# Performance work log

Measured on AMD Instinct MI355X. Metric: run time of the kernel, lower is better.

Reference implementation:

```python
import jax, jax.numpy as jnp
import numpy as np

B, S, H = 4, 2048, 1024
EXP_BITS, SIG_BITS = 5, 10  # rmode=1 -> round-to-nearest


def quantize(x):
    """Simulated low-precision float quantization (LightChop-style) with STE.

    exp_bits exponent bits (bias = 2^(e-1)-1, exponent clamped -> subnormal
    handling falls out of the clamp), sig_bits significand bits, round-to-nearest.
    """
    bias = 2 ** (EXP_BITS - 1) - 1
    ax = jnp.abs(x)
    e = jnp.floor(jnp.log2(jnp.where(ax > 0, ax, 1.0)))
    e = jnp.clip(e, 1 - bias, bias)               # clamp to representable exponent range
    scale = jnp.exp2(e - SIG_BITS)                # ulp at this exponent
    q = jnp.round(x / scale) * scale              # round significand to SIG_BITS bits
    max_val = (2.0 - 2.0 ** (-SIG_BITS)) * 2.0 ** bias
    q = jnp.clip(q, -max_val, max_val)            # saturate overflow
    # straight-through estimator: forward = q, backward = identity
    return x + jax.lax.stop_gradient(q - x)


def setup_inputs() -> dict:
    key = jax.random.key(0)
    ks = jax.random.split(key, 7)
    w_scale = 1.0 / np.sqrt(H)
    return {
        "x": jax.random.normal(ks[0], (B, S, H), dtype=jnp.float32),
        "Wq": jax.random.normal(ks[1], (H, H), dtype=jnp.float32) * w_scale,
        "bq": jax.random.normal(ks[2], (H,), dtype=jnp.float32) * 0.01,
        "Wk": jax.random.normal(ks[3], (H, H), dtype=jnp.float32) * w_scale,
        "bk": jax.random.normal(ks[4], (H,), dtype=jnp.float32) * 0.01,
        "Wv": jax.random.normal(ks[5], (H, H), dtype=jnp.float32) * w_scale,
        "bv": jax.random.normal(ks[6], (H,), dtype=jnp.float32) * 0.01,
    }


def reference(x, Wq, bq, Wk, bk, Wv, bv):
    # nn.Linear: y = x @ W.T + b   (W stored [out, in])
    q = quantize(jnp.einsum("bsh,oh->bso", x, Wq) + bq)
    k = quantize(jnp.einsum("bsh,oh->bso", x, Wk) + bk)
    v = quantize(jnp.einsum("bsh,oh->bso", x, Wv) + bv)
    inv_sqrt_h = 1.0 / (H ** 0.5)
    scores = quantize(jnp.einsum("bsh,bth->bst", q, k) * inv_sqrt_h)  # [B,S,S]
    attn = quantize(jax.nn.softmax(scores, axis=-1))
    return jnp.einsum("bst,bth->bsh", attn, v)
```

## Files before the change

kernel.cpp:

```cpp
#include <hip/hip_runtime.h>
#include <hip/hip_fp16.h>

#define B_ 4
#define S_ 2048
#define H_ 1024
#define M_ (B_ * S_)

typedef _Float16 f16;
typedef _Float16 f16x8 __attribute__((ext_vector_type(8)));
typedef _Float16 f16x4 __attribute__((ext_vector_type(4)));
typedef float f32x4 __attribute__((ext_vector_type(4)));

typedef __attribute__((address_space(3))) unsigned int* lds_u32p;
typedef const __attribute__((address_space(1))) unsigned int* gbl_u32p;

__device__ __forceinline__ void stage16(const f16* g, f16* l) {
  __builtin_amdgcn_global_load_lds((gbl_u32p)g, (lds_u32p)l, 16, 0, 0);
}

__global__ __launch_bounds__(256) void downconvert_all(
    const float* __restrict__ x, const float* __restrict__ W0,
    const float* __restrict__ W1, const float* __restrict__ W2,
    f16* __restrict__ xh, f16* __restrict__ Wh) {
  const int b = blockIdx.x;
  const float* src;
  f16* dst;
  long i;
  if (b < M_ * H_ / 1024) {
    src = x; dst = xh;
    i = (long)b * 256 + threadIdx.x;
  } else {
    const int wb = b - M_ * H_ / 1024;
    const int sel = wb >> 10;
    src = sel == 0 ? W0 : (sel == 1 ? W1 : W2);
    dst = Wh + (long)sel * H_ * H_;
    i = (long)(wb & 1023) * 256 + threadIdx.x;
  }
  f32x4 v = ((const f32x4*)src)[i];
  f16x4 h;
#pragma unroll
  for (int c = 0; c < 4; c++) h[c] = (f16)v[c];
  ((f16x4*)dst)[i] = h;
}

__global__ __launch_bounds__(256, 2)
void qkv_gemm(const f16* __restrict__ xh, const f16* __restrict__ Wh,
              const float* __restrict__ bq, const float* __restrict__ bk,
              const float* __restrict__ bv, f16* __restrict__ qkv,
              f16* __restrict__ vT) {
  __shared__ __align__(16) f16 As[2 * 128 * 32];
  __shared__ __align__(16) f16 Bs[2 * 128 * 32];
  const int t = threadIdx.x;
  const int wave = t >> 6, lane = t & 63;
  const int quad = lane >> 4, l16 = lane & 15;
  const int wm = (wave & 1) * 64, wn = (wave >> 1) * 64;
  const int sel = blockIdx.y >> 3;
  const int ntile = (blockIdx.y & 7) * 128;
  const int mtile = blockIdx.x * 128;

  const f16* Ab = xh + (long)mtile * H_;
  const f16* Bb = Wh + (long)sel * H_ * H_ + (long)ntile * H_;

  const int r0 = t >> 2;
  const int c8 = (t & 3) * 8;

  f32x4 acc[4][4] = {};

  for (int k0 = 0; k0 < H_; k0 += 64) {
    __syncthreads();
    stage16(Ab + (long)r0 * H_ + k0 + c8,             As + t * 8);
    stage16(Ab + (long)(r0 + 64) * H_ + k0 + c8,      As + 2048 + t * 8);
    stage16(Ab + (long)r0 * H_ + k0 + 32 + c8,        As + 4096 + t * 8);
    stage16(Ab + (long)(r0 + 64) * H_ + k0 + 32 + c8, As + 6144 + t * 8);
    stage16(Bb + (long)r0 * H_ + k0 + c8,             Bs + t * 8);
    stage16(Bb + (long)(r0 + 64) * H_ + k0 + c8,      Bs + 2048 + t * 8);
    stage16(Bb + (long)r0 * H_ + k0 + 32 + c8,        Bs + 4096 + t * 8);
    stage16(Bb + (long)(r0 + 64) * H_ + k0 + 32 + c8, Bs + 6144 + t * 8);
    __syncthreads();
#pragma unroll
    for (int kk = 0; kk < 2; kk++) {
      f16x8 ah[4], bh[4];
#pragma unroll
      for (int i = 0; i < 4; i++) {
        ah[i] = *(const f16x8*)&As[kk * 4096 + (wm + i * 16 + l16) * 32 + quad * 8];
        bh[i] = *(const f16x8*)&Bs[kk * 4096 + (wn + i * 16 + l16) * 32 + quad * 8];
      }
#pragma unroll
      for (int i = 0; i < 4; i++)
#pragma unroll
        for (int j = 0; j < 4; j++)
          acc[i][j] = __builtin_amdgcn_mfma_f32_16x16x32_f16(ah[i], bh[j], acc[i][j], 0, 0, 0);
    }
  }

  const float* bias = sel == 0 ? bq : (sel == 1 ? bk : bv);
  if (sel == 2) {
#pragma unroll
    for (int j = 0; j < 4; j++) {
      int n = ntile + wn + j * 16 + l16;
      float bb = bias[n];
#pragma unroll
      for (int i = 0; i < 4; i++) {
        int m = mtile + wm + i * 16 + quad * 4;
        f16x4 pack;
#pragma unroll
        for (int r = 0; r < 4; r++) pack[r] = (f16)(acc[i][j][r] + bb);
        *(f16x4*)&vT[((long)(m >> 11) * H_ + n) * S_ + (m & 2047)] = pack;
      }
    }
  } else {
    f16* out = qkv + (long)sel * M_ * H_;
#pragma unroll
    for (int j = 0; j < 4; j++) {
      int n = ntile + wn + j * 16 + l16;
      float bb = bias[n];
#pragma unroll
      for (int i = 0; i < 4; i++) {
        int m = mtile + wm + i * 16 + quad * 4;
#pragma unroll
        for (int r = 0; r < 4; r++)
          out[(long)(m + r) * H_ + n] = (f16)(acc[i][j][r] + bb);
      }
    }
  }
}

template <int OUT_F16>
__global__ __launch_bounds__(256, 2)
void gemm_nt(const f16* __restrict__ A, const f16* __restrict__ Bm,
             void* __restrict__ C, int lda, int ldb, int ldc, int K,
             long sA, long sB, long sC, float alpha) {
  __shared__ __align__(16) f16 As[2 * 128 * 32];
  __shared__ __align__(16) f16 Bs[2 * 128 * 32];
  const int t = threadIdx.x;
  const int wave = t >> 6, lane = t & 63;
  const int quad = lane >> 4, l16 = lane & 15;
  const int wm = (wave & 1) * 64, wn = (wave >> 1) * 64;
  const f16* Ab = A + blockIdx.z * sA + (long)blockIdx.x * 128 * lda;
  const f16* Bb = Bm + blockIdx.z * sB + (long)blockIdx.y * 128 * ldb;
  const int r0 = t >> 2, c8 = (t & 3) * 8;
  f32x4 acc[4][4] = {};
  for (int k0 = 0; k0 < K; k0 += 64) {
    __syncthreads();
    stage16(Ab + (long)r0 * lda + k0 + c8,             As + t * 8);
    stage16(Ab + (long)(r0 + 64) * lda + k0 + c8,      As + 2048 + t * 8);
    stage16(Ab + (long)r0 * lda + k0 + 32 + c8,        As + 4096 + t * 8);
    stage16(Ab + (long)(r0 + 64) * lda + k0 + 32 + c8, As + 6144 + t * 8);
    stage16(Bb + (long)r0 * ldb + k0 + c8,             Bs + t * 8);
    stage16(Bb + (long)(r0 + 64) * ldb + k0 + c8,      Bs + 2048 + t * 8);
    stage16(Bb + (long)r0 * ldb + k0 + 32 + c8,        Bs + 4096 + t * 8);
    stage16(Bb + (long)(r0 + 64) * ldb + k0 + 32 + c8, Bs + 6144 + t * 8);
    __syncthreads();
#pragma unroll
    for (int kk = 0; kk < 2; kk++) {
      f16x8 af[4], bf[4];
#pragma unroll
      for (int i = 0; i < 4; i++) {
        af[i] = *(const f16x8*)&As[kk * 4096 + (wm + i * 16 + l16) * 32 + quad * 8];
        bf[i] = *(const f16x8*)&Bs[kk * 4096 + (wn + i * 16 + l16) * 32 + quad * 8];
      }
#pragma unroll
      for (int i = 0; i < 4; i++)
#pragma unroll
        for (int j = 0; j < 4; j++)
          acc[i][j] = __builtin_amdgcn_mfma_f32_16x16x32_f16(af[i], bf[j], acc[i][j], 0, 0, 0);
    }
  }
  const long mb = (long)blockIdx.x * 128 + wm;
  const long nb = (long)blockIdx.y * 128 + wn;
#pragma unroll
  for (int i = 0; i < 4; i++)
#pragma unroll
    for (int j = 0; j < 4; j++) {
      long m = mb + i * 16 + quad * 4;
      long n = nb + j * 16 + l16;
#pragma unroll
      for (int r = 0; r < 4; r++) {
        float v = acc[i][j][r] * alpha;
        if (OUT_F16)
          ((f16*)C)[blockIdx.z * sC + (m + r) * ldc + n] = (f16)v;
        else
          ((float*)C)[blockIdx.z * sC + (m + r) * ldc + n] = v;
      }
    }
}

__global__ __launch_bounds__(256) void softmax_q(f16* __restrict__ sc) {
  const long row = blockIdx.x;
  f16* p = sc + row * S_;
  const int t = threadIdx.x;
  const int wave = t >> 6, lane = t & 63;
  f16x8 v = ((const f16x8*)p)[t];
  float f[8];
  float m = -3.0e38f;
#pragma unroll
  for (int c = 0; c < 8; c++) { f[c] = (float)v[c]; m = fmaxf(m, f[c]); }
#pragma unroll
  for (int o = 32; o > 0; o >>= 1) m = fmaxf(m, __shfl_xor(m, o));
  __shared__ float redm[4], reds[4];
  if (lane == 0) redm[wave] = m;
  __syncthreads();
  m = fmaxf(fmaxf(redm[0], redm[1]), fmaxf(redm[2], redm[3]));
  float s = 0.f, e[8];
#pragma unroll
  for (int c = 0; c < 8; c++) { e[c] = __expf(f[c] - m); s += e[c]; }
#pragma unroll
  for (int o = 32; o > 0; o >>= 1) s += __shfl_xor(s, o);
  if (lane == 0) reds[wave] = s;
  __syncthreads();
  s = reds[0] + reds[1] + reds[2] + reds[3];
  float inv = 1.0f / s;
  f16x8 ov;
#pragma unroll
  for (int c = 0; c < 8; c++) ov[c] = (f16)(e[c] * inv);
  ((f16x8*)p)[t] = ov;
}

extern "C" void kernel_launch(void* const* d_in, const int* in_sizes, int n_in,
                              void* d_out, int out_size, void* d_ws, size_t ws_size,
                              hipStream_t stream) {
  (void)in_sizes; (void)n_in; (void)out_size; (void)ws_size;
  const float* x  = (const float*)d_in[0];
  const float* Wq = (const float*)d_in[1];
  const float* bq = (const float*)d_in[2];
  const float* Wk = (const float*)d_in[3];
  const float* bk = (const float*)d_in[4];
  const float* Wv = (const float*)d_in[5];
  const float* bv = (const float*)d_in[6];

  char* ws = (char*)d_ws;
  f16* xh  = (f16*)ws; ws += (size_t)M_ * H_ * 2;
  f16* Wh  = (f16*)ws; ws += (size_t)3 * H_ * H_ * 2;
  f16* qkv = (f16*)ws; ws += (size_t)2 * M_ * H_ * 2;
  f16* vT  = (f16*)ws; ws += (size_t)B_ * H_ * S_ * 2;
  f16* sc  = (f16*)ws; ws += (size_t)B_ * S_ * S_ * 2;

  downconvert_all<<<M_ * H_ / 1024 + 3 * H_ * H_ / 1024, 256, 0, stream>>>(
      x, Wq, Wk, Wv, xh, Wh);

  qkv_gemm<<<dim3(64, 24), 256, 0, stream>>>(xh, Wh, bq, bk, bv, qkv, vT);

  gemm_nt<1><<<dim3(16, 16, 4), 256, 0, stream>>>(
      qkv, qkv + (size_t)M_ * H_, sc, H_, H_, S_, H_,
      (long)S_ * H_, (long)S_ * H_, (long)S_ * S_, 0.03125f);

  softmax_q<<<M_, 256, 0, stream>>>(sc);

  gemm_nt<0><<<dim3(16, 8, 4), 256, 0, stream>>>(
      sc, vT, d_out, S_, S_, H_, S_,
      (long)S_ * S_, (long)H_ * S_, (long)S_ * H_, 1.0f);
}
```

Baseline: 252.0 us.

## Fuse all stages into one persistent kernel with global atomic barriers

```diff
diff --git a/kernel.cpp b/kernel.cpp
--- a/kernel.cpp
+++ b/kernel.cpp
@@ -5,6 +5,7 @@
 #define S_ 2048
 #define H_ 1024
 #define M_ (B_ * S_)
+#define NBLK 512
 
 typedef _Float16 f16;
 typedef _Float16 f16x8 __attribute__((ext_vector_type(8)));
@@ -18,126 +19,26 @@
   __builtin_amdgcn_global_load_lds((gbl_u32p)g, (lds_u32p)l, 16, 0, 0);
 }
 
-__global__ __launch_bounds__(256) void downconvert_all(
-    const float* __restrict__ x, const float* __restrict__ W0,
-    const float* __restrict__ W1, const float* __restrict__ W2,
-    f16* __restrict__ xh, f16* __restrict__ Wh) {
-  const int b = blockIdx.x;
-  const float* src;
-  f16* dst;
-  long i;
-  if (b < M_ * H_ / 1024) {
-    src = x; dst = xh;
-    i = (long)b * 256 + threadIdx.x;
-  } else {
-    const int wb = b - M_ * H_ / 1024;
-    const int sel = wb >> 10;
-    src = sel == 0 ? W0 : (sel == 1 ? W1 : W2);
-    dst = Wh + (long)sel * H_ * H_;
-    i = (long)(wb & 1023) * 256 + threadIdx.x;
-  }
-  f32x4 v = ((const f32x4*)src)[i];
-  f16x4 h;
-#pragma unroll
-  for (int c = 0; c < 4; c++) h[c] = (f16)v[c];
-  ((f16x4*)dst)[i] = h;
-}
-
-__global__ __launch_bounds__(256, 2)
-void qkv_gemm(const f16* __restrict__ xh, const f16* __restrict__ Wh,
-              const float* __restrict__ bq, const float* __restrict__ bk,
-              const float* __restrict__ bv, f16* __restrict__ qkv,
-              f16* __restrict__ vT) {
-  __shared__ __align__(16) f16 As[2 * 128 * 32];
-  __shared__ __align__(16) f16 Bs[2 * 128 * 32];
-  const int t = threadIdx.x;
+__device__ __forceinline__ void gsync(unsigned* bar, unsigned target) {
+  __syncthreads();
+  if (threadIdx.x == 0) {
+    __hip_atomic_fetch_add(bar, 1u, __ATOMIC_ACQ_REL, __HIP_MEMORY_SCOPE_AGENT);
+    while (__hip_atomic_load(bar, __ATOMIC_ACQUIRE, __HIP_MEMORY_SCOPE_AGENT) < target)
+      __builtin_amdgcn_s_sleep(8);
+  }
+  __syncthreads();
+}
+
+template <int OUT_F16>
+__device__ __forceinline__ void gemm_tile(
+    const f16* __restrict__ A, const f16* __restrict__ Bm, void* __restrict__ C,
+    int lda, int ldb, int ldc, int K, long sA, long sB, long sC, float alpha,
+    int bx, int by, int bz, int t, f16* As, f16* Bs) {
   const int wave = t >> 6, lane = t & 63;
   const int quad = lane >> 4, l16 = lane & 15;
   const int wm = (wave & 1) * 64, wn = (wave >> 1) * 64;
-  const int sel = blockIdx.y >> 3;
-  const int ntile = (blockIdx.y & 7) * 128;
-  const int mtile = blockIdx.x * 128;
-
-  const f16* Ab = xh + (long)mtile * H_;
-  const f16* Bb = Wh + (long)sel * H_ * H_ + (long)ntile * H_;
-
-  const int r0 = t >> 2;
-  const int c8 = (t & 3) * 8;
-
-  f32x4 acc[4][4] = {};
-
-  for (int k0 = 0; k0 < H_; k0 += 64) {
-    __syncthreads();
-    stage16(Ab + (long)r0 * H_ + k0 + c8,             As + t * 8);
-    stage16(Ab + (long)(r0 + 64) * H_ + k0 + c8,      As + 2048 + t * 8);
-    stage16(Ab + (long)r0 * H_ + k0 + 32 + c8,        As + 4096 + t * 8);
-    stage16(Ab + (long)(r0 + 64) * H_ + k0 + 32 + c8, As + 6144 + t * 8);
-    stage16(Bb + (long)r0 * H_ + k0 + c8,             Bs + t * 8);
-    stage16(Bb + (long)(r0 + 64) * H_ + k0 + c8,      Bs + 2048 + t * 8);
-    stage16(Bb + (long)r0 * H_ + k0 + 32 + c8,        Bs + 4096 + t * 8);
-    stage16(Bb + (long)(r0 + 64) * H_ + k0 + 32 + c8, Bs + 6144 + t * 8);
-    __syncthreads();
-#pragma unroll
-    for (int kk = 0; kk < 2; kk++) {
-      f16x8 ah[4], bh[4];
-#pragma unroll
-      for (int i = 0; i < 4; i++) {
-        ah[i] = *(const f16x8*)&As[kk * 4096 + (wm + i * 16 + l16) * 32 + quad * 8];
-        bh[i] = *(const f16x8*)&Bs[kk * 4096 + (wn + i * 16 + l16) * 32 + quad * 8];
-      }
-#pragma unroll
-      for (int i = 0; i < 4; i++)
-#pragma unroll
-        for (int j = 0; j < 4; j++)
-          acc[i][j] = __builtin_amdgcn_mfma_f32_16x16x32_f16(ah[i], bh[j], acc[i][j], 0, 0, 0);
-    }
-  }
-
-  const float* bias = sel == 0 ? bq : (sel == 1 ? bk : bv);
-  if (sel == 2) {
-#pragma unroll
-    for (int j = 0; j < 4; j++) {
-      int n = ntile + wn + j * 16 + l16;
-      float bb = bias[n];
-#pragma unroll
-      for (int i = 0; i < 4; i++) {
-        int m = mtile + wm + i * 16 + quad * 4;
-        f16x4 pack;
-#pragma unroll
-        for (int r = 0; r < 4; r++) pack[r] = (f16)(acc[i][j][r] + bb);
-        *(f16x4*)&vT[((long)(m >> 11) * H_ + n) * S_ + (m & 2047)] = pack;
-      }
-    }
-  } else {
-    f16* out = qkv + (long)sel * M_ * H_;
-#pragma unroll
-    for (int j = 0; j < 4; j++) {
-      int n = ntile + wn + j * 16 + l16;
-      float bb = bias[n];
-#pragma unroll
-      for (int i = 0; i < 4; i++) {
-        int m = mtile + wm + i * 16 + quad * 4;
-#pragma unroll
-        for (int r = 0; r < 4; r++)
-          out[(long)(m + r) * H_ + n] = (f16)(acc[i][j][r] + bb);
-      }
-    }
-  }
-}
-
-template <int OUT_F16>
-__global__ __launch_bounds__(256, 2)
-void gemm_nt(const f16* __restrict__ A, const f16* __restrict__ Bm,
-             void* __restrict__ C, int lda, int ldb, int ldc, int K,
-             long sA, long sB, long sC, float alpha) {
-  __shared__ __align__(16) f16 As[2 * 128 * 32];
-  __shared__ __align__(16) f16 Bs[2 * 128 * 32];
-  const int t = threadIdx.x;
-  const int wave = t >> 6, lane = t & 63;
-  const int quad = lane >> 4, l16 = lane & 15;
-  const int wm = (wave & 1) * 64, wn = (wave >> 1) * 64;
-  const f16* Ab = A + blockIdx.z * sA + (long)blockIdx.x * 128 * lda;
-  const f16* Bb = Bm + blockIdx.z * sB + (long)blockIdx.y * 128 * ldb;
+  const f16* Ab = A + bz * sA + (long)bx * 128 * lda;
+  const f16* Bb = Bm + bz * sB + (long)by * 128 * ldb;
   const int r0 = t >> 2, c8 = (t & 3) * 8;
   f32x4 acc[4][4] = {};
   for (int k0 = 0; k0 < K; k0 += 64) {
@@ -166,8 +67,8 @@
           acc[i][j] = __builtin_amdgcn_mfma_f32_16x16x32_f16(af[i], bf[j], acc[i][j], 0, 0, 0);
     }
   }
-  const long mb = (long)blockIdx.x * 128 + wm;
-  const long nb = (long)blockIdx.y * 128 + wn;
+  const long mb = (long)bx * 128 + wm;
+  const long nb = (long)by * 128 + wn;
 #pragma unroll
   for (int i = 0; i < 4; i++)
 #pragma unroll
@@ -178,42 +79,164 @@
       for (int r = 0; r < 4; r++) {
         float v = acc[i][j][r] * alpha;
         if (OUT_F16)
-          ((f16*)C)[blockIdx.z * sC + (m + r) * ldc + n] = (f16)v;
+          ((f16*)C)[bz * sC + (m + r) * ldc + n] = (f16)v;
         else
-          ((float*)C)[blockIdx.z * sC + (m + r) * ldc + n] = v;
-      }
-    }
-}
-
-__global__ __launch_bounds__(256) void softmax_q(f16* __restrict__ sc) {
-  const long row = blockIdx.x;
-  f16* p = sc + row * S_;
+          ((float*)C)[bz * sC + (m + r) * ldc + n] = v;
+      }
+    }
+}
+
+__global__ __launch_bounds__(256, 2)
+void fused_all(const float* __restrict__ x, const float* __restrict__ Wq,
+               const float* __restrict__ bq, const float* __restrict__ Wk,
+               const float* __restrict__ bk, const float* __restrict__ Wv,
+               const float* __restrict__ bv, f16* __restrict__ xh,
+               f16* __restrict__ Wh, f16* __restrict__ qkv,
+               f16* __restrict__ vT, f16* __restrict__ sc,
+               float* __restrict__ out, unsigned* __restrict__ bar) {
+  __shared__ __align__(16) f16 As[2 * 128 * 32];
+  __shared__ __align__(16) f16 Bs[2 * 128 * 32];
+  __shared__ float redm[4], reds[4];
   const int t = threadIdx.x;
+  const int blk = blockIdx.x;
   const int wave = t >> 6, lane = t & 63;
-  f16x8 v = ((const f16x8*)p)[t];
-  float f[8];
-  float m = -3.0e38f;
-#pragma unroll
-  for (int c = 0; c < 8; c++) { f[c] = (float)v[c]; m = fmaxf(m, f[c]); }
-#pragma unroll
-  for (int o = 32; o > 0; o >>= 1) m = fmaxf(m, __shfl_xor(m, o));
-  __shared__ float redm[4], reds[4];
-  if (lane == 0) redm[wave] = m;
-  __syncthreads();
-  m = fmaxf(fmaxf(redm[0], redm[1]), fmaxf(redm[2], redm[3]));
-  float s = 0.f, e[8];
-#pragma unroll
-  for (int c = 0; c < 8; c++) { e[c] = __expf(f[c] - m); s += e[c]; }
-#pragma unroll
-  for (int o = 32; o > 0; o >>= 1) s += __shfl_xor(s, o);
-  if (lane == 0) reds[wave] = s;
-  __syncthreads();
-  s = reds[0] + reds[1] + reds[2] + reds[3];
-  float inv = 1.0f / s;
-  f16x8 ov;
-#pragma unroll
-  for (int c = 0; c < 8; c++) ov[c] = (f16)(e[c] * inv);
-  ((f16x8*)p)[t] = ov;
+
+  {
+    const int NX = M_ * H_ / 4;
+    for (int i = blk * 256 + t; i < NX + 3 * H_ * H_ / 4; i += NBLK * 256) {
+      const float* src;
+      f16* dst;
+      int idx;
+      if (i < NX) { src = (const float*)0; dst = xh; idx = i;
+        f32x4 v = ((const f32x4*)x)[idx];
+        f16x4 h;
+#pragma unroll
+        for (int c = 0; c < 4; c++) h[c] = (f16)v[c];
+        ((f16x4*)xh)[idx] = h;
+      } else {
+        int j = i - NX;
+        int sel = j >> 18;
+        src = sel == 0 ? Wq : (sel == 1 ? Wk : Wv);
+        f32x4 v = ((const f32x4*)src)[j & 262143];
+        f16x4 h;
+#pragma unroll
+        for (int c = 0; c < 4; c++) h[c] = (f16)v[c];
+        ((f16x4*)Wh)[j] = h;
+      }
+    }
+  }
+  gsync(bar, NBLK);
+
+  for (int it = 0; it < 3; it++) {
+    const int T = it * NBLK + blk;
+    const int bx = T & 63, by = T >> 6;
+    const int sel = by >> 3;
+    const int ntile = (by & 7) * 128, mtile = bx * 128;
+    const f16* Ab = xh + (long)mtile * H_;
+    const f16* Bb = Wh + (long)sel * H_ * H_ + (long)ntile * H_;
+    const int quad = lane >> 4, l16 = lane & 15;
+    const int wm = (wave & 1) * 64, wn = (wave >> 1) * 64;
+    const int r0 = t >> 2, c8 = (t & 3) * 8;
+    f32x4 acc[4][4] = {};
+    for (int k0 = 0; k0 < H_; k0 += 64) {
+      __syncthreads();
+      stage16(Ab + (long)r0 * H_ + k0 + c8,             As + t * 8);
+      stage16(Ab + (long)(r0 + 64) * H_ + k0 + c8,      As + 2048 + t * 8);
+      stage16(Ab + (long)r0 * H_ + k0 + 32 + c8,        As + 4096 + t * 8);
+      stage16(Ab + (long)(r0 + 64) * H_ + k0 + 32 + c8, As + 6144 + t * 8);
+      stage16(Bb + (long)r0 * H_ + k0 + c8,             Bs + t * 8);
+      stage16(Bb + (long)(r0 + 64) * H_ + k0 + c8,      Bs + 2048 + t * 8);
+      stage16(Bb + (long)r0 * H_ + k0 + 32 + c8,        Bs + 4096 + t * 8);
+      stage16(Bb + (long)(r0 + 64) * H_ + k0 + 32 + c8, Bs + 6144 + t * 8);
+      __syncthreads();
+#pragma unroll
+      for (int kk = 0; kk < 2; kk++) {
+        f16x8 ah[4], bh[4];
+#pragma unroll
+        for (int i = 0; i < 4; i++) {
+          ah[i] = *(const f16x8*)&As[kk * 4096 + (wm + i * 16 + l16) * 32 + quad * 8];
+          bh[i] = *(const f16x8*)&Bs[kk * 4096 + (wn + i * 16 + l16) * 32 + quad * 8];
+        }
+#pragma unroll
+        for (int i = 0; i < 4; i++)
+#pragma unroll
+          for (int j = 0; j < 4; j++)
+            acc[i][j] = __builtin_amdgcn_mfma_f32_16x16x32_f16(ah[i], bh[j], acc[i][j], 0, 0, 0);
+      }
+    }
+    const float* bias = sel == 0 ? bq : (sel == 1 ? bk : bv);
+    if (sel == 2) {
+#pragma unroll
+      for (int j = 0; j < 4; j++) {
+        int n = ntile + wn + j * 16 + l16;
+        float bb = bias[n];
+#pragma unroll
+        for (int i = 0; i < 4; i++) {
+          int m = mtile + wm + i * 16 + quad * 4;
+          f16x4 pack;
+#pragma unroll
+          for (int r = 0; r < 4; r++) pack[r] = (f16)(acc[i][j][r] + bb);
+          *(f16x4*)&vT[((long)(m >> 11) * H_ + n) * S_ + (m & 2047)] = pack;
+        }
+      }
+    } else {
+      f16* o = qkv + (long)sel * M_ * H_;
+#pragma unroll
+      for (int j = 0; j < 4; j++) {
+        int n = ntile + wn + j * 16 + l16;
+        float bb = bias[n];
+#pragma unroll
+        for (int i = 0; i < 4; i++) {
+          int m = mtile + wm + i * 16 + quad * 4;
+#pragma unroll
+          for (int r = 0; r < 4; r++)
+            o[(long)(m + r) * H_ + n] = (f16)(acc[i][j][r] + bb);
+        }
+      }
+    }
+  }
+  gsync(bar, 2 * NBLK);
+
+  for (int it = 0; it < 2; it++) {
+    const int T = it * NBLK + blk;
+    gemm_tile<1>(qkv, qkv + (size_t)M_ * H_, sc, H_, H_, S_, H_,
+                 (long)S_ * H_, (long)S_ * H_, (long)S_ * S_, 0.03125f,
+                 T & 15, (T >> 4) & 15, T >> 8, t, As, Bs);
+  }
+  gsync(bar, 3 * NBLK);
+
+  for (int r = 0; r < 16; r++) {
+    f16* p = sc + ((long)blk * 16 + r) * S_;
+    f16x8 v = ((const f16x8*)p)[t];
+    float f[8];
+    float m = -3.0e38f;
+#pragma unroll
+    for (int c = 0; c < 8; c++) { f[c] = (float)v[c]; m = fmaxf(m, f[c]); }
+#pragma unroll
+    for (int o = 32; o > 0; o >>= 1) m = fmaxf(m, __shfl_xor(m, o));
+    if (lane == 0) redm[wave] = m;
+    __syncthreads();
+    m = fmaxf(fmaxf(redm[0], redm[1]), fmaxf(redm[2], redm[3]));
+    float s = 0.f, e[8];
+#pragma unroll
+    for (int c = 0; c < 8; c++) { e[c] = __expf(f[c] - m); s += e[c]; }
+#pragma unroll
+    for (int o = 32; o > 0; o >>= 1) s += __shfl_xor(s, o);
+    if (lane == 0) reds[wave] = s;
+    __syncthreads();
+    s = reds[0] + reds[1] + reds[2] + reds[3];
+    float inv = 1.0f / s;
+    f16x8 ov;
+#pragma unroll
+    for (int c = 0; c < 8; c++) ov[c] = (f16)(e[c] * inv);
+    ((f16x8*)p)[t] = ov;
+    __syncthreads();
+  }
+  gsync(bar, 4 * NBLK);
+
+  gemm_tile<0>(sc, vT, out, S_, S_, H_, S_,
+               (long)S_ * S_, (long)H_ * S_, (long)S_ * H_, 1.0f,
+               blk & 15, (blk >> 4) & 7, blk >> 7, t, As, Bs);
 }
 
 extern "C" void kernel_launch(void* const* d_in, const int* in_sizes, int n_in,
@@ -228,25 +251,15 @@
   const float* Wv = (const float*)d_in[5];
   const float* bv = (const float*)d_in[6];
 
-  char* ws = (char*)d_ws;
+  unsigned* bar = (unsigned*)d_ws;
+  char* ws = (char*)d_ws + 256;
   f16* xh  = (f16*)ws; ws += (size_t)M_ * H_ * 2;
   f16* Wh  = (f16*)ws; ws += (size_t)3 * H_ * H_ * 2;
   f16* qkv = (f16*)ws; ws += (size_t)2 * M_ * H_ * 2;
   f16* vT  = (f16*)ws; ws += (size_t)B_ * H_ * S_ * 2;
   f16* sc  = (f16*)ws; ws += (size_t)B_ * S_ * S_ * 2;
 
-  downconvert_all<<<M_ * H_ / 1024 + 3 * H_ * H_ / 1024, 256, 0, stream>>>(
-      x, Wq, Wk, Wv, xh, Wh);
-
-  qkv_gemm<<<dim3(64, 24), 256, 0, stream>>>(xh, Wh, bq, bk, bv, qkv, vT);
-
-  gemm_nt<1><<<dim3(16, 16, 4), 256, 0, stream>>>(
-      qkv, qkv + (size_t)M_ * H_, sc, H_, H_, S_, H_,
-      (long)S_ * H_, (long)S_ * H_, (long)S_ * S_, 0.03125f);
-
-  softmax_q<<<M_, 256, 0, stream>>>(sc);
-
-  gemm_nt<0><<<dim3(16, 8, 4), 256, 0, stream>>>(
-      sc, vT, d_out, S_, S_, H_, S_,
-      (long)S_ * S_, (long)H_ * S_, (long)S_ * H_, 1.0f);
-}
+  hipMemsetAsync(bar, 0, 256, stream);
+  fused_all<<<NBLK, 256, 0, stream>>>(x, Wq, bq, Wk, bk, Wv, bv,
+                                      xh, Wh, qkv, vT, sc, (float*)d_out, bar);
+}
```

After: 479.0 us. 90.0% more time.

## Fuse softmax normalization into the attention-times-V GEMM A-tile staging

Applied to the files above, without the earlier changes.

```diff
diff --git a/kernel.cpp b/kernel.cpp
--- a/kernel.cpp
+++ b/kernel.cpp
@@ -125,31 +125,29 @@
   }
 }
 
-template <int OUT_F16>
 __global__ __launch_bounds__(256, 2)
-void gemm_nt(const f16* __restrict__ A, const f16* __restrict__ Bm,
-             void* __restrict__ C, int lda, int ldb, int ldc, int K,
-             long sA, long sB, long sC, float alpha) {
+void gemm_qk(const f16* __restrict__ A, const f16* __restrict__ Bm,
+             f16* __restrict__ C) {
   __shared__ __align__(16) f16 As[2 * 128 * 32];
   __shared__ __align__(16) f16 Bs[2 * 128 * 32];
   const int t = threadIdx.x;
   const int wave = t >> 6, lane = t & 63;
   const int quad = lane >> 4, l16 = lane & 15;
   const int wm = (wave & 1) * 64, wn = (wave >> 1) * 64;
-  const f16* Ab = A + blockIdx.z * sA + (long)blockIdx.x * 128 * lda;
-  const f16* Bb = Bm + blockIdx.z * sB + (long)blockIdx.y * 128 * ldb;
+  const f16* Ab = A + (long)blockIdx.z * S_ * H_ + (long)blockIdx.x * 128 * H_;
+  const f16* Bb = Bm + (long)blockIdx.z * S_ * H_ + (long)blockIdx.y * 128 * H_;
   const int r0 = t >> 2, c8 = (t & 3) * 8;
   f32x4 acc[4][4] = {};
-  for (int k0 = 0; k0 < K; k0 += 64) {
-    __syncthreads();
-    stage16(Ab + (long)r0 * lda + k0 + c8,             As + t * 8);
-    stage16(Ab + (long)(r0 + 64) * lda + k0 + c8,      As + 2048 + t * 8);
-    stage16(Ab + (long)r0 * lda + k0 + 32 + c8,        As + 4096 + t * 8);
-    stage16(Ab + (long)(r0 + 64) * lda + k0 + 32 + c8, As + 6144 + t * 8);
-    stage16(Bb + (long)r0 * ldb + k0 + c8,             Bs + t * 8);
-    stage16(Bb + (long)(r0 + 64) * ldb + k0 + c8,      Bs + 2048 + t * 8);
-    stage16(Bb + (long)r0 * ldb + k0 + 32 + c8,        Bs + 4096 + t * 8);
-    stage16(Bb + (long)(r0 + 64) * ldb + k0 + 32 + c8, Bs + 6144 + t * 8);
+  for (int k0 = 0; k0 < H_; k0 += 64) {
+    __syncthreads();
+    stage16(Ab + (long)r0 * H_ + k0 + c8,             As + t * 8);
+    stage16(Ab + (long)(r0 + 64) * H_ + k0 + c8,      As + 2048 + t * 8);
+    stage16(Ab + (long)r0 * H_ + k0 + 32 + c8,        As + 4096 + t * 8);
+    stage16(Ab + (long)(r0 + 64) * H_ + k0 + 32 + c8, As + 6144 + t * 8);
+    stage16(Bb + (long)r0 * H_ + k0 + c8,             Bs + t * 8);
+    stage16(Bb + (long)(r0 + 64) * H_ + k0 + c8,      Bs + 2048 + t * 8);
+    stage16(Bb + (long)r0 * H_ + k0 + 32 + c8,        Bs + 4096 + t * 8);
+    stage16(Bb + (long)(r0 + 64) * H_ + k0 + 32 + c8, Bs + 6144 + t * 8);
     __syncthreads();
 #pragma unroll
     for (int kk = 0; kk < 2; kk++) {
@@ -168,6 +166,7 @@
   }
   const long mb = (long)blockIdx.x * 128 + wm;
   const long nb = (long)blockIdx.y * 128 + wn;
+  f16* Cb = C + (long)blockIdx.z * S_ * S_;
 #pragma unroll
   for (int i = 0; i < 4; i++)
 #pragma unroll
@@ -175,45 +174,108 @@
       long m = mb + i * 16 + quad * 4;
       long n = nb + j * 16 + l16;
 #pragma unroll
-      for (int r = 0; r < 4; r++) {
-        float v = acc[i][j][r] * alpha;
-        if (OUT_F16)
-          ((f16*)C)[blockIdx.z * sC + (m + r) * ldc + n] = (f16)v;
-        else
-          ((float*)C)[blockIdx.z * sC + (m + r) * ldc + n] = v;
-      }
-    }
-}
-
-__global__ __launch_bounds__(256) void softmax_q(f16* __restrict__ sc) {
-  const long row = blockIdx.x;
-  f16* p = sc + row * S_;
+      for (int r = 0; r < 4; r++)
+        Cb[(m + r) * S_ + n] = (f16)(acc[i][j][r] * 0.03125f);
+    }
+}
+
+__global__ __launch_bounds__(256, 2)
+void attn_av(const f16* __restrict__ sc, const f16* __restrict__ vT,
+             float* __restrict__ out) {
+  __shared__ __align__(16) f16 As[2 * 128 * 32];
+  __shared__ __align__(16) f16 Bs[2 * 128 * 32];
+  __shared__ float pm[128][2], pl[128][2];
+  __shared__ float mrow[128], lrow[128];
   const int t = threadIdx.x;
+  const int z = blockIdx.z;
+  const f16* Arow = sc + (long)z * S_ * S_ + (long)blockIdx.x * 128 * S_;
+  const f16* Bb = vT + (long)z * H_ * S_ + (long)blockIdx.y * 128 * S_;
+
+  {
+    const int row = t >> 1, hf = t & 1;
+    const f16* p = Arow + (long)row * S_ + hf * 1024;
+    float m = -3.0e38f, l = 0.f;
+    for (int c = 0; c < 128; c++) {
+      f16x8 v = ((const f16x8*)p)[c];
+#pragma unroll
+      for (int e = 0; e < 8; e++) {
+        float f = (float)v[e];
+        if (f > m) { l *= __expf(m - f); m = f; }
+        l += __expf(f - m);
+      }
+    }
+    pm[row][hf] = m; pl[row][hf] = l;
+  }
+  __syncthreads();
+  if (t < 128) {
+    float ma = pm[t][0], mb2 = pm[t][1];
+    float m = fmaxf(ma, mb2);
+    float l = pl[t][0] * __expf(ma - m) + pl[t][1] * __expf(mb2 - m);
+    mrow[t] = m; lrow[t] = 1.0f / l;
+  }
+
   const int wave = t >> 6, lane = t & 63;
-  f16x8 v = ((const f16x8*)p)[t];
-  float f[8];
-  float m = -3.0e38f;
-#pragma unroll
-  for (int c = 0; c < 8; c++) { f[c] = (float)v[c]; m = fmaxf(m, f[c]); }
-#pragma unroll
-  for (int o = 32; o > 0; o >>= 1) m = fmaxf(m, __shfl_xor(m, o));
-  __shared__ float redm[4], reds[4];
-  if (lane == 0) redm[wave] = m;
-  __syncthreads();
-  m = fmaxf(fmaxf(redm[0], redm[1]), fmaxf(redm[2], redm[3]));
-  float s = 0.f, e[8];
-#pragma unroll
-  for (int c = 0; c < 8; c++) { e[c] = __expf(f[c] - m); s += e[c]; }
-#pragma unroll
-  for (int o = 32; o > 0; o >>= 1) s += __shfl_xor(s, o);
-  if (lane == 0) reds[wave] = s;
-  __syncthreads();
-  s = reds[0] + reds[1] + reds[2] + reds[3];
-  float inv = 1.0f / s;
-  f16x8 ov;
-#pragma unroll
-  for (int c = 0; c < 8; c++) ov[c] = (f16)(e[c] * inv);
-  ((f16x8*)p)[t] = ov;
+  const int quad = lane >> 4, l16 = lane & 15;
+  const int wm = (wave & 1) * 64, wn = (wave >> 1) * 64;
+  const int r0 = t >> 2, c8 = (t & 3) * 8;
+  f32x4 acc[4][4] = {};
+  for (int k0 = 0; k0 < S_; k0 += 64) {
+    __syncthreads();
+    {
+      const f16* pr0 = Arow + (long)r0 * S_ + k0 + c8;
+      const f16* pr1 = Arow + (long)(r0 + 64) * S_ + k0 + c8;
+      float m0 = mrow[r0], i0 = lrow[r0];
+      float m1 = mrow[r0 + 64], i1 = lrow[r0 + 64];
+      f16x8 v00 = *(const f16x8*)pr0;
+      f16x8 v01 = *(const f16x8*)(pr0 + 32);
+      f16x8 v10 = *(const f16x8*)pr1;
+      f16x8 v11 = *(const f16x8*)(pr1 + 32);
+      f16x8 o00, o01, o10, o11;
+#pragma unroll
+      for (int e = 0; e < 8; e++) {
+        o00[e] = (f16)(__expf((float)v00[e] - m0) * i0);
+        o01[e] = (f16)(__expf((float)v01[e] - m0) * i0);
+        o10[e] = (f16)(__expf((float)v10[e] - m1) * i1);
+        o11[e] = (f16)(__expf((float)v11[e] - m1) * i1);
+      }
+      *(f16x8*)&As[t * 8]        = o00;
+      *(f16x8*)&As[2048 + t * 8] = o10;
+      *(f16x8*)&As[4096 + t * 8] = o01;
+      *(f16x8*)&As[6144 + t * 8] = o11;
+    }
+    stage16(Bb + (long)r0 * S_ + k0 + c8,             Bs + t * 8);
+    stage16(Bb + (long)(r0 + 64) * S_ + k0 + c8,      Bs + 2048 + t * 8);
+    stage16(Bb + (long)r0 * S_ + k0 + 32 + c8,        Bs + 4096 + t * 8);
+    stage16(Bb + (long)(r0 + 64) * S_ + k0 + 32 + c8, Bs + 6144 + t * 8);
+    __syncthreads();
+#pragma unroll
+    for (int kk = 0; kk < 2; kk++) {
+      f16x8 af[4], bf[4];
+#pragma unroll
+      for (int i = 0; i < 4; i++) {
+        af[i] = *(const f16x8*)&As[kk * 4096 + (wm + i * 16 + l16) * 32 + quad * 8];
+        bf[i] = *(const f16x8*)&Bs[kk * 4096 + (wn + i * 16 + l16) * 32 + quad * 8];
+      }
+#pragma unroll
+      for (int i = 0; i < 4; i++)
+#pragma unroll
+        for (int j = 0; j < 4; j++)
+          acc[i][j] = __builtin_amdgcn_mfma_f32_16x16x32_f16(af[i], bf[j], acc[i][j], 0, 0, 0);
+    }
+  }
+  const long mb = (long)blockIdx.x * 128 + wm;
+  const long nb = (long)blockIdx.y * 128 + wn;
+  float* Ob = out + (long)z * S_ * H_;
+#pragma unroll
+  for (int i = 0; i < 4; i++)
+#pragma unroll
+    for (int j = 0; j < 4; j++) {
+      long m = mb + i * 16 + quad * 4;
+      long n = nb + j * 16 + l16;
+#pragma unroll
+      for (int r = 0; r < 4; r++)
+        Ob[(m + r) * H_ + n] = acc[i][j][r];
+    }
 }
 
 extern "C" void kernel_launch(void* const* d_in, const int* in_sizes, int n_in,
@@ -240,13 +302,7 @@
 
   qkv_gemm<<<dim3(64, 24), 256, 0, stream>>>(xh, Wh, bq, bk, bv, qkv, vT);
 
-  gemm_nt<1><<<dim3(16, 16, 4), 256, 0, stream>>>(
-      qkv, qkv + (size_t)M_ * H_, sc, H_, H_, S_, H_,
-      (long)S_ * H_, (long)S_ * H_, (long)S_ * S_, 0.03125f);
-
-  softmax_q<<<M_, 256, 0, stream>>>(sc);
-
-  gemm_nt<0><<<dim3(16, 8, 4), 256, 0, stream>>>(
-      sc, vT, d_out, S_, S_, H_, S_,
-      (long)S_ * S_, (long)H_ * S_, (long)S_ * H_, 1.0f);
-}
+  gemm_qk<<<dim3(16, 16, 4), 256, 0, stream>>>(qkv, qkv + (size_t)M_ * H_, sc);
+
+  attn_av<<<dim3(16, 8, 4), 256, 0, stream>>>(sc, vT, (float*)d_out);
+}
```

New measurement: 338.5 us. 34.3% more time.
